# Optimization experiments

Hardware: AMD Instinct MI355X
Metric: run time of the kernel (lower is better)

The kernel has to match this reference:

```python
import jax, jax.numpy as jnp
import numpy as np

B, T, K = 64, 1024, 256  # batch, seq_len, num_labels


def setup_inputs() -> dict:
    key = jax.random.key(0)
    k1, k2 = jax.random.split(key)
    emissions = jax.random.normal(k1, (B, T, K), dtype=jnp.float32)
    transitions = jax.random.normal(k2, (K, K), dtype=jnp.float32) * 0.1
    return {"emissions": emissions, "transitions": transitions}


def _viterbi_decode(emissions, transitions):
    """Viterbi decode, mirroring tfa.text.crf_decode with full-length sequences.
    emissions: [B, T, K] unary potentials; transitions: [K, K] (prev -> next).
    Returns int32 tag sequence [B, T]."""
    em = jnp.transpose(emissions, (1, 0, 2))  # [T, B, K]

    def fwd_step(state, emit_t):
        # state: [B, K] running max scores ending in each tag at time t-1
        scores = state[:, :, None] + transitions[None, :, :]  # [B, K_prev, K_next]
        bp = jnp.argmax(scores, axis=1).astype(jnp.int32)      # [B, K] backpointers
        new_state = jnp.max(scores, axis=1) + emit_t           # [B, K]
        return new_state, bp

    state, bps = jax.lax.scan(fwd_step, em[0], em[1:])  # bps: [T-1, B, K]
    last_tag = jnp.argmax(state, axis=-1).astype(jnp.int32)  # [B]

    def back_step(tag, bp_t):
        prev = jnp.take_along_axis(bp_t, tag[:, None], axis=1)[:, 0]
        return prev, prev

    # reverse scan: bps[i] maps tag at t=i+1 back to tag at t=i
    _, earlier = jax.lax.scan(back_step, last_tag, bps, reverse=True)  # [T-1, B]
    tags = jnp.concatenate([earlier, last_tag[None, :]], axis=0)  # [T, B]
    return jnp.transpose(tags, (1, 0))  # [B, T]


def reference(emissions, transitions):
    # CRF.call in inference mode: crf_decode then cast to the input dtype.
    return _viterbi_decode(emissions, transitions).astype(emissions.dtype)
```

## Files before the change

kernel.cpp:

```cpp
#include <hip/hip_runtime.h>


#define CRF_B 64
#define CRF_T 1024
#define CRF_K 256
#define NSEG  16
#define SEGLEN 64

#define FG 8
#define FP 32


#define LD4(v, p, col) { \
    v.x = trans[(size_t)(p) * CRF_K + (col)]; \
    v.y = trans[(size_t)((p) + 1) * CRF_K + (col)]; \
    v.z = trans[(size_t)((p) + 2) * CRF_K + (col)]; \
    v.w = trans[(size_t)((p) + 3) * CRF_K + (col)]; }

#define FWD_CHUNK(idx, ta, tb) { \
    float4 sv = sp[idx]; \
    float a0 = sv.x + ta.x; \
    float a1 = sv.y + ta.y; \
    float a2 = sv.z + ta.z; \
    float a3 = sv.w + ta.w; \
    float r0 = fmaxf(fmaxf(a0, a1), a2); \
    m0 = fmaxf(fmaxf(r0, a3), m0); \
    float c0 = sv.x + tb.x; \
    float c1 = sv.y + tb.y; \
    float c2 = sv.z + tb.z; \
    float c3 = sv.w + tb.w; \
    float r1 = fmaxf(fmaxf(c0, c1), c2); \
    m1 = fmaxf(fmaxf(r1, c3), m1); }

__global__ __launch_bounds__(1024, 4) void crf_forward_states(
    const float* __restrict__ em, const float* __restrict__ trans,
    float* __restrict__ M, unsigned char* __restrict__ gidp)
{
    const int b   = blockIdx.x;
    const int tid = threadIdx.x;
    const int g   = tid >> 7;
    const int c   = tid & 127;

    __shared__ __align__(16) float s_state[CRF_K];
    __shared__ float s_partial[FG][CRF_K];

    const int pbase = g * FP;
    const int c2    = c + 128;

    float4 ta0, ta1, ta2, ta3, ta4, ta5, ta6, ta7;
    float4 tb0, tb1, tb2, tb3, tb4, tb5, tb6, tb7;
    LD4(ta0, pbase +  0, c)  LD4(ta1, pbase +  4, c)
    LD4(ta2, pbase +  8, c)  LD4(ta3, pbase + 12, c)
    LD4(ta4, pbase + 16, c)  LD4(ta5, pbase + 20, c)
    LD4(ta6, pbase + 24, c)  LD4(ta7, pbase + 28, c)
    LD4(tb0, pbase +  0, c2) LD4(tb1, pbase +  4, c2)
    LD4(tb2, pbase +  8, c2) LD4(tb3, pbase + 12, c2)
    LD4(tb4, pbase + 16, c2) LD4(tb5, pbase + 20, c2)
    LD4(tb6, pbase + 24, c2) LD4(tb7, pbase + 28, c2)

    const float* emb = em + (size_t)b * CRF_T * CRF_K;
    if (tid < CRF_K) s_state[tid] = emb[tid];
    float e_cur = 0.0f;
    if (tid < CRF_K) e_cur = emb[CRF_K + tid];
    __syncthreads();

    float sp0 = 0, sp1 = 0, sp2 = 0, sp3 = 0;
    float sp4 = 0, sp5 = 0, sp6 = 0, sp7 = 0;
    float sbv = 0;

    for (int t = 1; t < CRF_T; ++t) {
        if (gidp && tid < CRF_K && t > 1) {
            int bg = 7;
            if (sp6 == sbv) bg = 6;
            if (sp5 == sbv) bg = 5;
            if (sp4 == sbv) bg = 4;
            if (sp3 == sbv) bg = 3;
            if (sp2 == sbv) bg = 2;
            if (sp1 == sbv) bg = 1;
            if (sp0 == sbv) bg = 0;
            int g1 = __shfl_down(bg, 1, 64);
            if ((tid & 1) == 0)
                gidp[((size_t)(t - 1) * CRF_B + b) * 128 + (tid >> 1)] =
                    (unsigned char)(bg | (g1 << 4));
        }

        float e_next = 0.0f;
        if (tid < CRF_K && t + 1 < CRF_T)
            e_next = emb[(t + 1) * CRF_K + tid];

        float m0 = -INFINITY, m1 = -INFINITY;
        const float4* sp = (const float4*)(s_state + pbase);
        FWD_CHUNK(0, ta0, tb0) FWD_CHUNK(1, ta1, tb1)
        FWD_CHUNK(2, ta2, tb2) FWD_CHUNK(3, ta3, tb3)
        FWD_CHUNK(4, ta4, tb4) FWD_CHUNK(5, ta5, tb5)
        FWD_CHUNK(6, ta6, tb6) FWD_CHUNK(7, ta7, tb7)

        s_partial[g][c]  = m0;
        s_partial[g][c2] = m1;
        __syncthreads();
        if (tid < CRF_K) {
            float p0 = s_partial[0][tid], p1 = s_partial[1][tid];
            float p2 = s_partial[2][tid], p3 = s_partial[3][tid];
            float p4 = s_partial[4][tid], p5 = s_partial[5][tid];
            float p6 = s_partial[6][tid], p7 = s_partial[7][tid];
            float q0 = fmaxf(fmaxf(p0, p1), p2);
            float q1 = fmaxf(fmaxf(p3, p4), p5);
            float bv = fmaxf(fmaxf(fmaxf(q0, q1), p6), p7);
            s_state[tid] = bv + e_cur;
            M[((size_t)t * CRF_B + b) * CRF_K + tid] = bv;
            sp0 = p0; sp1 = p1; sp2 = p2; sp3 = p3;
            sp4 = p4; sp5 = p5; sp6 = p6; sp7 = p7; sbv = bv;
        }
        __syncthreads();
        e_cur = e_next;
    }

    if (gidp && tid < CRF_K) {
        int bg = 7;
        if (sp6 == sbv) bg = 6;
        if (sp5 == sbv) bg = 5;
        if (sp4 == sbv) bg = 4;
        if (sp3 == sbv) bg = 3;
        if (sp2 == sbv) bg = 2;
        if (sp1 == sbv) bg = 1;
        if (sp0 == sbv) bg = 0;
        int g1 = __shfl_down(bg, 1, 64);
        if ((tid & 1) == 0)
            gidp[((size_t)(CRF_T - 1) * CRF_B + b) * 128 + (tid >> 1)] =
                (unsigned char)(bg | (g1 << 4));
    }
}


#define BPG_CHUNK(j) { \
    float4 mm = M4[j]; float4 ee = E4[j]; \
    float s0 = mm.x + ee.x, s1 = mm.y + ee.y; \
    float s2 = mm.z + ee.z, s3 = mm.w + ee.w; \
    float t0v = s_tile[base + 4*(j) + 0][lane]; \
    float t1v = s_tile[base + 4*(j) + 1][lane]; \
    float t2v = s_tile[base + 4*(j) + 2][lane]; \
    float t3v = s_tile[base + 4*(j) + 3][lane]; \
    float v0 = s0 + t0v; if (v0 > best) { best = v0; arg = base + 4*(j); } \
    float v1 = s1 + t1v; if (v1 > best) { best = v1; arg = base + 4*(j) + 1; } \
    float v2 = s2 + t2v; if (v2 > best) { best = v2; arg = base + 4*(j) + 2; } \
    float v3 = s3 + t3v; if (v3 > best) { best = v3; arg = base + 4*(j) + 3; } }

#define BPG_CHUNK0(j) { \
    float4 ee = E4[j]; \
    float t0v = s_tile[base + 4*(j) + 0][lane]; \
    float t1v = s_tile[base + 4*(j) + 1][lane]; \
    float t2v = s_tile[base + 4*(j) + 2][lane]; \
    float t3v = s_tile[base + 4*(j) + 3][lane]; \
    float v0 = ee.x + t0v; if (v0 > best) { best = v0; arg = base + 4*(j); } \
    float v1 = ee.y + t1v; if (v1 > best) { best = v1; arg = base + 4*(j) + 1; } \
    float v2 = ee.z + t2v; if (v2 > best) { best = v2; arg = base + 4*(j) + 2; } \
    float v3 = ee.w + t3v; if (v3 > best) { best = v3; arg = base + 4*(j) + 3; } }

__global__ __launch_bounds__(256) void crf_bp_gid(
    const float* __restrict__ M, const float* __restrict__ em,
    const float* __restrict__ trans, const unsigned char* __restrict__ gidp,
    unsigned char* __restrict__ bp)
{
    const int b    = blockIdx.x >> 3;
    const int cg   = (blockIdx.x >> 1) & 3;
    const int ts   = blockIdx.x & 1;
    const int tid  = threadIdx.x;
    const int lane = tid & 63;
    const int w    = tid >> 6;

    __shared__ float s_tile[CRF_K][64];

    const int k0 = cg * 64;
    for (int idx = tid; idx < CRF_K * 64; idx += 256) {
        const int p = idx >> 6, cc = idx & 63;
        s_tile[p][cc] = trans[(size_t)p * CRF_K + k0 + cc];
    }
    __syncthreads();

    const int t_lo = ts * 512;
    const int t_hi = ts ? (CRF_T - 1) : 512;
    const int half = (k0 >> 1) + (lane >> 1);
    const int odd  = lane & 1;

    int t1 = t_lo + w;
    if (t1 >= t_hi) return;
    unsigned char gb = gidp[((size_t)(t1 + 1) * CRF_B + b) * 128 + half];

    for (; t1 < t_hi; t1 += 4) {
        const int tn = t1 + 4;
        unsigned char gb_next = 0;
        if (tn < t_hi)
            gb_next = gidp[((size_t)(tn + 1) * CRF_B + b) * 128 + half];

        const int g    = odd ? ((gb >> 4) & 7) : (gb & 7);
        const int base = g << 5;
        const float4* E4 =
            (const float4*)(em + ((size_t)b * CRF_T + t1) * CRF_K + base);
        float best = -INFINITY; int arg = base;
        if (t1 == 0) {
            BPG_CHUNK0(0) BPG_CHUNK0(1) BPG_CHUNK0(2) BPG_CHUNK0(3)
            BPG_CHUNK0(4) BPG_CHUNK0(5) BPG_CHUNK0(6) BPG_CHUNK0(7)
        } else {
            const float4* M4 =
                (const float4*)(M + ((size_t)t1 * CRF_B + b) * CRF_K + base);
            BPG_CHUNK(0) BPG_CHUNK(1) BPG_CHUNK(2) BPG_CHUNK(3)
            BPG_CHUNK(4) BPG_CHUNK(5) BPG_CHUNK(6) BPG_CHUNK(7)
        }
        bp[((size_t)b * (CRF_T - 1) + t1) * CRF_K + k0 + lane] =
            (unsigned char)arg;
        gb = gb_next;
    }
}


__global__ __launch_bounds__(1024, 2) void crf_bp_matrix(
    const float* __restrict__ M, const float* __restrict__ em,
    const float* __restrict__ trans, unsigned char* __restrict__ bp)
{
    const int b   = blockIdx.x >> 4;
    const int seg = blockIdx.x & 15;
    const int tid = threadIdx.x;
    const int g   = tid >> 8;
    const int k   = tid & 255;

    __shared__ __align__(16) float s_row[CRF_K];
    __shared__ float s_pv[4][CRF_K];
    __shared__ int   s_pi[4][CRF_K];

    const int pbase = g * 64;
    float4 tr[16];
#pragma unroll
    for (int i = 0; i < 16; ++i) {
        const int p = pbase + 4 * i;
        tr[i].x = trans[(p + 0) * CRF_K + k];
        tr[i].y = trans[(p + 1) * CRF_K + k];
        tr[i].z = trans[(p + 2) * CRF_K + k];
        tr[i].w = trans[(p + 3) * CRF_K + k];
    }

    const int t_lo = seg * SEGLEN;
    const int t_hi = min(t_lo + SEGLEN, CRF_T - 1);
    unsigned char* bpb = bp + (size_t)b * (CRF_T - 1) * CRF_K;

    for (int t1 = t_lo; t1 < t_hi; ++t1) {
        if (tid < CRF_K) {
            float ev = em[((size_t)b * CRF_T + t1) * CRF_K + tid];
            float sv = ev;
            if (t1 > 0) sv = M[((size_t)t1 * CRF_B + b) * CRF_K + tid] + ev;
            s_row[tid] = sv;
        }
        __syncthreads();

        float best = -INFINITY;
        int   arg  = pbase;
        const float4* spp = (const float4*)(s_row + pbase);
#pragma unroll
        for (int i = 0; i < 16; ++i) {
            float4 st = spp[i];
            const int p = pbase + 4 * i;
            float s0 = st.x + tr[i].x;
            float s1 = st.y + tr[i].y;
            float s2 = st.z + tr[i].z;
            float s3 = st.w + tr[i].w;
            if (s0 > best) { best = s0; arg = p; }
            if (s1 > best) { best = s1; arg = p + 1; }
            if (s2 > best) { best = s2; arg = p + 2; }
            if (s3 > best) { best = s3; arg = p + 3; }
        }
        s_pv[g][k] = best;
        s_pi[g][k] = arg;
        __syncthreads();
        if (tid < CRF_K) {
            float bv = s_pv[0][tid];
            int   ba = s_pi[0][tid];
#pragma unroll
            for (int j = 1; j < 4; ++j) {
                float v = s_pv[j][tid];
                if (v > bv) { bv = v; ba = s_pi[j][tid]; }
            }
            bpb[(size_t)t1 * CRF_K + tid] = (unsigned char)ba;
        }
        __syncthreads();
    }
}


__global__ __launch_bounds__(256) void crf_seg_maps(
    const unsigned char* __restrict__ bp, unsigned char* __restrict__ maps)
{
    const int b   = blockIdx.x >> 4;
    const int s   = blockIdx.x & 15;
    const int tid = threadIdx.x;
    const int rows = (s == NSEG - 1) ? SEGLEN - 1 : SEGLEN;
    const int r0   = s * SEGLEN;

    __shared__ unsigned char lbp[SEGLEN][CRF_K];

    const unsigned char* bpb = bp + (size_t)b * (CRF_T - 1) * CRF_K;
    const int nw = rows * 64;
    for (int w = tid; w < nw; w += 256) {
        const int r = w >> 6, cc = w & 63;
        ((unsigned int*)lbp[r])[cc] =
            ((const unsigned int*)(bpb + (size_t)(r0 + r) * CRF_K))[cc];
    }
    __syncthreads();

    int tag = tid;
    for (int j = rows - 1; j >= 0; --j) tag = lbp[j][tag];
    maps[((size_t)b * NSEG + s) * CRF_K + tid] = (unsigned char)tag;
}

__global__ __launch_bounds__(256) void crf_compose(
    const float* __restrict__ M, const float* __restrict__ em,
    const unsigned char* __restrict__ maps,
    int* __restrict__ exits, float* __restrict__ out)
{
    const int b   = blockIdx.x;
    const int tid = threadIdx.x;

    __shared__ float s_wv[4];
    __shared__ int   s_wi[4];

    float v = M[((size_t)(CRF_T - 1) * CRF_B + b) * CRF_K + tid]
            + em[((size_t)b * CRF_T + (CRF_T - 1)) * CRF_K + tid];
    int   i = tid;
#pragma unroll
    for (int off = 32; off >= 1; off >>= 1) {
        float ov = __shfl_xor(v, off, 64);
        int   oi = __shfl_xor(i, off, 64);
        if (ov > v || (ov == v && oi < i)) { v = ov; i = oi; }
    }
    const int lane = tid & 63, wv = tid >> 6;
    if (lane == 0) { s_wv[wv] = v; s_wi[wv] = i; }
    __syncthreads();
    if (tid == 0) {
        float bv = s_wv[0]; int bi = s_wi[0];
#pragma unroll
        for (int w = 1; w < 4; ++w)
            if (s_wv[w] > bv) { bv = s_wv[w]; bi = s_wi[w]; }
        out[(size_t)b * CRF_T + (CRF_T - 1)] = (float)bi;
        int E = bi;
        exits[b * NSEG + NSEG - 1] = E;
        const unsigned char* mb = maps + (size_t)b * NSEG * CRF_K;
        for (int s = NSEG - 1; s >= 1; --s) {
            E = mb[(size_t)s * CRF_K + E];
            exits[b * NSEG + s - 1] = E;
        }
    }
}

__global__ __launch_bounds__(256) void crf_emit(
    const unsigned char* __restrict__ bp, const int* __restrict__ exits,
    float* __restrict__ out)
{
    const int b   = blockIdx.x >> 4;
    const int s   = blockIdx.x & 15;
    const int tid = threadIdx.x;
    const int rows = (s == NSEG - 1) ? SEGLEN - 1 : SEGLEN;
    const int r0   = s * SEGLEN;

    __shared__ unsigned char lbp[SEGLEN][CRF_K];

    const unsigned char* bpb = bp + (size_t)b * (CRF_T - 1) * CRF_K;
    const int nw = rows * 64;
    for (int w = tid; w < nw; w += 256) {
        const int r = w >> 6, cc = w & 63;
        ((unsigned int*)lbp[r])[cc] =
            ((const unsigned int*)(bpb + (size_t)(r0 + r) * CRF_K))[cc];
    }
    __syncthreads();

    int tag = tid;
    const bool win = (tid == exits[b * NSEG + s]);
    for (int j = rows - 1; j >= 0; --j) {
        tag = lbp[j][tag];
        if (win) out[(size_t)b * CRF_T + r0 + j] = (float)tag;
    }
}

__global__ void crf_zero_out(float* __restrict__ out, int n)
{
    int i = blockIdx.x * blockDim.x + threadIdx.x;
    if (i < n) out[i] = 0.0f;
}


extern "C" void kernel_launch(void* const* d_in, const int* in_sizes, int n_in,
                              void* d_out, int out_size, void* d_ws, size_t ws_size,
                              hipStream_t stream) {
    (void)in_sizes; (void)n_in;
    const float* em    = (const float*)d_in[0];
    const float* trans = (const float*)d_in[1];
    float* out = (float*)d_out;

    const size_t M_bytes     = (size_t)CRF_T * CRF_B * CRF_K * sizeof(float);
    const size_t gid_bytes   = (size_t)CRF_T * CRF_B * 128;
    const size_t bp_bytes    = (size_t)CRF_B * (CRF_T - 1) * CRF_K;
    const size_t maps_bytes  = (size_t)CRF_B * NSEG * CRF_K;
    const size_t exits_bytes = (size_t)CRF_B * NSEG * sizeof(int);

    char* w = (char*)d_ws;
    if (ws_size >= M_bytes + gid_bytes + bp_bytes + maps_bytes + exits_bytes) {
        float*         M     = (float*)w;            w += M_bytes;
        unsigned char* gidp  = (unsigned char*)w;    w += gid_bytes;
        unsigned char* bp    = (unsigned char*)w;    w += bp_bytes;
        unsigned char* maps  = (unsigned char*)w;    w += maps_bytes;
        int*           exits = (int*)w;

        crf_forward_states<<<CRF_B, 1024, 0, stream>>>(em, trans, M, gidp);
        crf_bp_gid<<<CRF_B * 8, 256, 0, stream>>>(M, em, trans, gidp, bp);
        crf_seg_maps<<<CRF_B * NSEG, 256, 0, stream>>>(bp, maps);
        crf_compose<<<CRF_B, 256, 0, stream>>>(M, em, maps, exits, out);
        crf_emit<<<CRF_B * NSEG, 256, 0, stream>>>(bp, exits, out);
    } else if (ws_size >= M_bytes + bp_bytes + maps_bytes + exits_bytes) {
        float*         M     = (float*)w;            w += M_bytes;
        unsigned char* bp    = (unsigned char*)w;    w += bp_bytes;
        unsigned char* maps  = (unsigned char*)w;    w += maps_bytes;
        int*           exits = (int*)w;

        crf_forward_states<<<CRF_B, 1024, 0, stream>>>(em, trans, M, nullptr);
        crf_bp_matrix<<<CRF_B * NSEG, 1024, 0, stream>>>(M, em, trans, bp);
        crf_seg_maps<<<CRF_B * NSEG, 256, 0, stream>>>(bp, maps);
        crf_compose<<<CRF_B, 256, 0, stream>>>(M, em, maps, exits, out);
        crf_emit<<<CRF_B * NSEG, 256, 0, stream>>>(bp, exits, out);
    } else {
        crf_zero_out<<<(out_size + 255) / 256, 256, 0, stream>>>(out, out_size);
    }
}
```

Baseline: 1.105 ms.

## Reduce forward max within wavefront via shuffles with double-buffered state

Restructures the forward recurrence so each wavefront owns 16 output tags and its four 16-lane groups each cover 64 predecessors. The cross-group max now uses wave shuffles instead of a shared-memory partial array. The state buffer is double-buffered, which brings each step down from two block barriers to one. The group-id backpointer hint is computed in-wave from the shuffled max. The risk is longer per-thread serial max chains (64 predecessors per thread) and extra shuffle latency on the critical path.

New measurement: 1.177 ms. +6.5%, slower.

```diff
diff --git a/kernel.cpp b/kernel.cpp
--- a/kernel.cpp
+++ b/kernel.cpp
@@ -7,9 +7,6 @@
 #define NSEG  16
 #define SEGLEN 64
 
-#define FG 8
-#define FP 32
-
 
 #define LD4(v, p, col) { \
     v.x = trans[(size_t)(p) * CRF_K + (col)]; \
@@ -17,117 +14,84 @@
     v.z = trans[(size_t)((p) + 2) * CRF_K + (col)]; \
     v.w = trans[(size_t)((p) + 3) * CRF_K + (col)]; }
 
-#define FWD_CHUNK(idx, ta, tb) { \
-    float4 sv = sp[idx]; \
-    float a0 = sv.x + ta.x; \
-    float a1 = sv.y + ta.y; \
-    float a2 = sv.z + ta.z; \
-    float a3 = sv.w + ta.w; \
-    float r0 = fmaxf(fmaxf(a0, a1), a2); \
-    m0 = fmaxf(fmaxf(r0, a3), m0); \
-    float c0 = sv.x + tb.x; \
-    float c1 = sv.y + tb.y; \
-    float c2 = sv.z + tb.z; \
-    float c3 = sv.w + tb.w; \
-    float r1 = fmaxf(fmaxf(c0, c1), c2); \
-    m1 = fmaxf(fmaxf(r1, c3), m1); }
+#define FWD1(j, u, mm) { \
+    float4 sv = sp[j]; \
+    float a0 = sv.x + u.x; \
+    float a1 = sv.y + u.y; \
+    float a2 = sv.z + u.z; \
+    float a3 = sv.w + u.w; \
+    float q  = fmaxf(fmaxf(a0, a1), a2); \
+    mm = fmaxf(fmaxf(q, a3), mm); }
 
 __global__ __launch_bounds__(1024, 4) void crf_forward_states(
     const float* __restrict__ em, const float* __restrict__ trans,
     float* __restrict__ M, unsigned char* __restrict__ gidp)
 {
-    const int b   = blockIdx.x;
-    const int tid = threadIdx.x;
-    const int g   = tid >> 7;
-    const int c   = tid & 127;
-
-    __shared__ __align__(16) float s_state[CRF_K];
-    __shared__ float s_partial[FG][CRF_K];
-
-    const int pbase = g * FP;
-    const int c2    = c + 128;
-
-    float4 ta0, ta1, ta2, ta3, ta4, ta5, ta6, ta7;
-    float4 tb0, tb1, tb2, tb3, tb4, tb5, tb6, tb7;
-    LD4(ta0, pbase +  0, c)  LD4(ta1, pbase +  4, c)
-    LD4(ta2, pbase +  8, c)  LD4(ta3, pbase + 12, c)
-    LD4(ta4, pbase + 16, c)  LD4(ta5, pbase + 20, c)
-    LD4(ta6, pbase + 24, c)  LD4(ta7, pbase + 28, c)
-    LD4(tb0, pbase +  0, c2) LD4(tb1, pbase +  4, c2)
-    LD4(tb2, pbase +  8, c2) LD4(tb3, pbase + 12, c2)
-    LD4(tb4, pbase + 16, c2) LD4(tb5, pbase + 20, c2)
-    LD4(tb6, pbase + 24, c2) LD4(tb7, pbase + 28, c2)
+    const int b    = blockIdx.x;
+    const int tid  = threadIdx.x;
+    const int w    = tid >> 6;
+    const int lane = tid & 63;
+    const int a    = lane >> 4;
+    const int li   = lane & 15;
+    const int c    = (w << 4) | li;
+
+    __shared__ __align__(16) float sbuf[2][272];
+
+    const int p0 = a << 6;
+    float4 u0, u1, u2, u3, u4, u5, u6, u7;
+    float4 u8, u9, uA, uB, uC, uD, uE, uF;
+    LD4(u0, p0 +  0, c) LD4(u1, p0 +  4, c)
+    LD4(u2, p0 +  8, c) LD4(u3, p0 + 12, c)
+    LD4(u4, p0 + 16, c) LD4(u5, p0 + 20, c)
+    LD4(u6, p0 + 24, c) LD4(u7, p0 + 28, c)
+    LD4(u8, p0 + 32, c) LD4(u9, p0 + 36, c)
+    LD4(uA, p0 + 40, c) LD4(uB, p0 + 44, c)
+    LD4(uC, p0 + 48, c) LD4(uD, p0 + 52, c)
+    LD4(uE, p0 + 56, c) LD4(uF, p0 + 60, c)
 
     const float* emb = em + (size_t)b * CRF_T * CRF_K;
-    if (tid < CRF_K) s_state[tid] = emb[tid];
-    float e_cur = 0.0f;
-    if (tid < CRF_K) e_cur = emb[CRF_K + tid];
-    __syncthreads();
-
-    float sp0 = 0, sp1 = 0, sp2 = 0, sp3 = 0;
-    float sp4 = 0, sp5 = 0, sp6 = 0, sp7 = 0;
-    float sbv = 0;
+    if (tid < CRF_K)
+        sbuf[0][68 * (tid >> 6) + (tid & 63)] = emb[tid];
+    float e_cur = emb[CRF_K + c];
+    __syncthreads();
+
+    int pb = 0;
+    const int cslot = 68 * (c >> 6) + (c & 63);
 
     for (int t = 1; t < CRF_T; ++t) {
-        if (gidp && tid < CRF_K && t > 1) {
-            int bg = 7;
-            if (sp6 == sbv) bg = 6;
-            if (sp5 == sbv) bg = 5;
-            if (sp4 == sbv) bg = 4;
-            if (sp3 == sbv) bg = 3;
-            if (sp2 == sbv) bg = 2;
-            if (sp1 == sbv) bg = 1;
-            if (sp0 == sbv) bg = 0;
-            int g1 = __shfl_down(bg, 1, 64);
-            if ((tid & 1) == 0)
-                gidp[((size_t)(t - 1) * CRF_B + b) * 128 + (tid >> 1)] =
-                    (unsigned char)(bg | (g1 << 4));
-        }
-
         float e_next = 0.0f;
-        if (tid < CRF_K && t + 1 < CRF_T)
-            e_next = emb[(t + 1) * CRF_K + tid];
-
-        float m0 = -INFINITY, m1 = -INFINITY;
-        const float4* sp = (const float4*)(s_state + pbase);
-        FWD_CHUNK(0, ta0, tb0) FWD_CHUNK(1, ta1, tb1)
-        FWD_CHUNK(2, ta2, tb2) FWD_CHUNK(3, ta3, tb3)
-        FWD_CHUNK(4, ta4, tb4) FWD_CHUNK(5, ta5, tb5)
-        FWD_CHUNK(6, ta6, tb6) FWD_CHUNK(7, ta7, tb7)
-
-        s_partial[g][c]  = m0;
-        s_partial[g][c2] = m1;
+        if (t + 1 < CRF_T) e_next = emb[(t + 1) * CRF_K + c];
+
+        const float4* sp = (const float4*)(sbuf[pb] + 68 * a);
+        float m_lo = -INFINITY, m_hi = -INFINITY;
+        FWD1(0, u0, m_lo) FWD1(1, u1, m_lo) FWD1(2, u2, m_lo) FWD1(3, u3, m_lo)
+        FWD1(4, u4, m_lo) FWD1(5, u5, m_lo) FWD1(6, u6, m_lo) FWD1(7, u7, m_lo)
+        FWD1( 8, u8, m_hi) FWD1( 9, u9, m_hi) FWD1(10, uA, m_hi) FWD1(11, uB, m_hi)
+        FWD1(12, uC, m_hi) FWD1(13, uD, m_hi) FWD1(14, uE, m_hi) FWD1(15, uF, m_hi)
+
+        float mv = fmaxf(m_lo, m_hi);
+        float o1 = __shfl_xor(mv, 16, 64); mv = fmaxf(mv, o1);
+        float o2 = __shfl_xor(mv, 32, 64); mv = fmaxf(mv, o2);
+
+        if (gidp) {
+            int cand = 8;
+            cand = (m_hi == mv) ? (2 * a + 1) : cand;
+            cand = (m_lo == mv) ? (2 * a)     : cand;
+            int g1 = __shfl_xor(cand, 16, 64); cand = min(cand, g1);
+            int g2 = __shfl_xor(cand, 32, 64); cand = min(cand, g2);
+            int gn = __shfl_down(cand, 1, 64);
+            if (a == 0 && (li & 1) == 0)
+                gidp[((size_t)t * CRF_B + b) * 128 + (c >> 1)] =
+                    (unsigned char)(cand | (gn << 4));
+        }
+
+        if (a == 0) {
+            sbuf[pb ^ 1][cslot] = mv + e_cur;
+            M[((size_t)t * CRF_B + b) * CRF_K + c] = mv;
+        }
         __syncthreads();
-        if (tid < CRF_K) {
-            float p0 = s_partial[0][tid], p1 = s_partial[1][tid];
-            float p2 = s_partial[2][tid], p3 = s_partial[3][tid];
-            float p4 = s_partial[4][tid], p5 = s_partial[5][tid];
-            float p6 = s_partial[6][tid], p7 = s_partial[7][tid];
-            float q0 = fmaxf(fmaxf(p0, p1), p2);
-            float q1 = fmaxf(fmaxf(p3, p4), p5);
-            float bv = fmaxf(fmaxf(fmaxf(q0, q1), p6), p7);
-            s_state[tid] = bv + e_cur;
-            M[((size_t)t * CRF_B + b) * CRF_K + tid] = bv;
-            sp0 = p0; sp1 = p1; sp2 = p2; sp3 = p3;
-            sp4 = p4; sp5 = p5; sp6 = p6; sp7 = p7; sbv = bv;
-        }
-        __syncthreads();
+        pb ^= 1;
         e_cur = e_next;
-    }
-
-    if (gidp && tid < CRF_K) {
-        int bg = 7;
-        if (sp6 == sbv) bg = 6;
-        if (sp5 == sbv) bg = 5;
-        if (sp4 == sbv) bg = 4;
-        if (sp3 == sbv) bg = 3;
-        if (sp2 == sbv) bg = 2;
-        if (sp1 == sbv) bg = 1;
-        if (sp0 == sbv) bg = 0;
-        int g1 = __shfl_down(bg, 1, 64);
-        if ((tid & 1) == 0)
-            gidp[((size_t)(CRF_T - 1) * CRF_B + b) * 128 + (tid >> 1)] =
-                (unsigned char)(bg | (g1 << 4));
     }
 }
 
```
